# Kernel optimization log

Hardware: AMD Instinct MI355X
Metric: run time of the kernel (lower is better)

## Reference

```python
import jax, jax.numpy as jnp
import numpy as np

SEQ, H, VOCAB = 2048, 1024, 32000

def setup_inputs() -> dict:
    key = jax.random.key(0)
    ks = jax.random.split(key, 13)
    s = lambda k, shape, fan: jax.random.normal(k, shape, dtype=jnp.float32) / np.sqrt(fan)
    return {
        "word_input": jax.random.randint(ks[0], (1,), 0, VOCAB, dtype=jnp.int64),
        "last_context": s(ks[1], (1, H), H),
        "last_hidden": s(ks[2], (1, H), H),
        "encoder_outputs": s(ks[3], (SEQ, H), H),
        "emb": s(ks[4], (VOCAB, H), H),
        "W_ih": s(ks[5], (4 * H, 2 * H), 2 * H),
        "W_hh": s(ks[6], (4 * H, H), H),
        "b_ih": s(ks[7], (4 * H,), H),
        "b_hh": s(ks[8], (4 * H,), H),
        "Wa": s(ks[9], (H, H), H),
        "ba": s(ks[10], (H,), H),
        "Wl": s(ks[11], (VOCAB, 2 * H), 2 * H),
        "bl": s(ks[12], (VOCAB,), 2 * H),
    }

def reference(word_input, last_context, last_hidden, encoder_outputs,
              emb, W_ih, W_hh, b_ih, b_hh, Wa, ba, Wl, bl):
    # embedding lookup (batch=1, single step): [H]
    x = emb[word_input[0]]
    # rnn_input = cat(embedded, last_context): [2H]
    inp = jnp.concatenate([x, last_context[0]])
    h0 = last_hidden[0]
    c0 = jnp.zeros_like(h0)
    # single LSTM step, PyTorch gate order (i, f, g, o)
    gates = W_ih @ inp + b_ih + W_hh @ h0 + b_hh  # [4H]
    i_g, f_g, g_g, o_g = jnp.split(gates, 4)
    c = jax.nn.sigmoid(f_g) * c0 + jax.nn.sigmoid(i_g) * jnp.tanh(g_g)
    h = jax.nn.sigmoid(o_g) * jnp.tanh(c)  # lstm_output, [H]
    # Bahdanau-style scores: dot(h, Wa @ enc_i + ba) for each position (vectorized)
    energies = (encoder_outputs @ Wa.T + ba) @ h  # [SEQ]
    attn_w = jax.nn.softmax(energies)
    context = attn_w @ encoder_outputs  # [H]
    logits = Wl @ jnp.concatenate([h, context]) + bl  # [VOCAB]
    out = jax.nn.log_softmax(logits)
    return out[None, :]  # [1, VOCAB]
```

## Files before the change

### kernel.cpp

```cpp
#include <hip/hip_runtime.h>
#include <hip/hip_bf16.h>
#include <math.h>

#define SEQ   2048
#define H     1024
#define VOCAB 32000
#define GRID2 2048
#define NTHR  256

__device__ inline float4 ld4(const float* p) { return *reinterpret_cast<const float4*>(p); }
typedef float vfloat4 __attribute__((ext_vector_type(4)));
__device__ inline float4 ld4nt(const float* p) {
    vfloat4 v = __builtin_nontemporal_load(reinterpret_cast<const vfloat4*>(p));
    return make_float4(v.x, v.y, v.z, v.w);
}
__device__ inline float dot4(float4 a, float4 b) { return a.x*b.x + a.y*b.y + a.z*b.z + a.w*b.w; }
__device__ inline float sigmoidf(float x) { return 1.f / (1.f + expf(-x)); }

__device__ inline void omerge(float& m, float& s, float m2, float s2) {
    if (m2 > m) { s = s * __expf(m - m2) + s2; m = m2; }
    else if (s2 != 0.f) { s += s2 * __expf(m2 - m); }
}
__device__ inline float waveSum(float v) {
#pragma unroll
    for (int off = 32; off > 0; off >>= 1) v += __shfl_down(v, off, 64);
    return v;
}
__device__ inline void waveOmerge(float& m, float& s) {
#pragma unroll
    for (int off = 32; off > 0; off >>= 1) {
        float m2 = __shfl_down(m, off, 64), ss = __shfl_down(s, off, 64);
        omerge(m, s, m2, ss);
    }
}

__device__ inline void blockSignal(unsigned* f) {
    __syncthreads();
    if (threadIdx.x == 0) {
        __threadfence();
        __hip_atomic_fetch_add(f, 1u, __ATOMIC_RELEASE, __HIP_MEMORY_SCOPE_AGENT);
    }
}
__device__ inline void blockWait(unsigned* f, unsigned target) {
    if (threadIdx.x == 0) {
        while (__hip_atomic_load(f, __ATOMIC_ACQUIRE, __HIP_MEMORY_SCOPE_AGENT) < target)
            __builtin_amdgcn_s_sleep(4);
        __threadfence();
    }
    __syncthreads();
}


__global__ __launch_bounds__(NTHR) void k_init(float* __restrict__ ws) {
    const int t = threadIdx.x;
    unsigned* fl = (unsigned*)ws;
    if (t < 128) fl[t] = 0u;
    float* ctx = ws + 1152;
    float* u   = ws + 2176;
    for (int k = t; k < H; k += NTHR) { u[k] = 0.f; ctx[k] = 0.f; }
}

__global__ __launch_bounds__(NTHR, 8) void k_main(
        const float* __restrict__ emb,  const float* __restrict__ lctx,
        const float* __restrict__ h0,   const float* __restrict__ W_ih,
        const float* __restrict__ W_hh, const float* __restrict__ b_ih,
        const float* __restrict__ b_hh, const int* __restrict__ widx,
        const float* __restrict__ enc,  const float* __restrict__ Wa,
        const float* __restrict__ Wl,   const float* __restrict__ bl,
        float* __restrict__ ws, float* __restrict__ out) {
    const int bid = blockIdx.x, t = threadIdx.x;
    const int wid = t >> 6, lane = t & 63;

    unsigned* f_h   = (unsigned*)ws + 0;
    unsigned* f_u   = (unsigned*)ws + 16;
    unsigned* f_e   = (unsigned*)ws + 32;
    unsigned* f_ctx = (unsigned*)ws + 48;
    unsigned* f_l   = (unsigned*)ws + 64;
    float*  vcat   = ws + 128;
    float*  h      = vcat;
    float*  ctx    = vcat + H;
    float*  u      = ws + 2176;
    float*  energ  = ws + 3200;
    float2* part_e = (float2*)(ws + 5248);
    float2* part_l = (float2*)(ws + 5760);

    __shared__ float  lg[12];
    __shared__ float  shh[16];
    __shared__ float  se[8];
    __shared__ float  shw[32];
    __shared__ float2 s2[4];

    if (bid < 1024) {
        const int j = bid;
        const int w = widx[0];
        const float* xep = emb + (size_t)w * H;
        const float* wi = W_ih + (size_t)j * (2 * H);
        const float* wg = W_ih + (size_t)(j + 2 * H) * (2 * H);
        const float* wo = W_ih + (size_t)(j + 3 * H) * (2 * H);
        const float* vi = W_hh + (size_t)j * H;
        const float* vg = W_hh + (size_t)(j + 2 * H) * H;
        const float* vo = W_hh + (size_t)(j + 3 * H) * H;
        const int e = t * 4;
        float4 x0 = ld4(xep + e), x1 = ld4(lctx + e), x2 = ld4(h0 + e);
        float ai = dot4(ld4nt(wi + e), x0) + dot4(ld4nt(wi + H + e), x1) + dot4(ld4nt(vi + e), x2);
        float ag = dot4(ld4nt(wg + e), x0) + dot4(ld4nt(wg + H + e), x1) + dot4(ld4nt(vg + e), x2);
        float ao = dot4(ld4nt(wo + e), x0) + dot4(ld4nt(wo + H + e), x1) + dot4(ld4nt(vo + e), x2);
        ai = waveSum(ai); ag = waveSum(ag); ao = waveSum(ao);
        if (lane == 0) { lg[wid*3] = ai; lg[wid*3+1] = ag; lg[wid*3+2] = ao; }
        __syncthreads();
        if (t == 0) {
            float gi = 0.f, gg = 0.f, go = 0.f;
            for (int q = 0; q < 4; ++q) { gi += lg[q*3]; gg += lg[q*3+1]; go += lg[q*3+2]; }
            gi += b_ih[j] + b_hh[j];
            gg += b_ih[j + 2*H] + b_hh[j + 2*H];
            go += b_ih[j + 3*H] + b_hh[j + 3*H];
            float c = sigmoidf(gi) * tanhf(gg);
            h[j] = sigmoidf(go) * tanhf(c);
        }
        blockSignal(f_h);
    }

    blockWait(f_h, 1024);

    if (bid >= 1024 && bid < 1280) {
        const int ab = bid - 1024;
        {
            const int rg = ab >> 2, kb = ab & 3;
            if (t < 16) shh[t] = h[rg * 16 + t];
            __syncthreads();
            const int k = kb * 256 + t;
            float acc = 0.f;
#pragma unroll
            for (int jj = 0; jj < 16; ++jj)
                acc += Wa[(size_t)(rg * 16 + jj) * H + k] * shh[jj];
            atomicAdd(&u[k], acc);
            blockSignal(f_u);
            blockWait(f_u, 256);
        }
        {
#pragma unroll
            for (int rr = 0; rr < 2; ++rr) {
                const int row = ab * 8 + wid * 2 + rr;
                const float* er = enc + (size_t)row * H;
                float acc = 0.f;
#pragma unroll
                for (int it = 0; it < 4; ++it) {
                    const int e = it * 256 + lane * 4;
                    acc += dot4(ld4(er + e), ld4(u + e));
                }
                acc = waveSum(acc);
                if (lane == 0) { energ[row] = acc; se[wid * 2 + rr] = acc; }
            }
            __syncthreads();
            if (t == 0) {
                float m = -INFINITY, s = 0.f;
                for (int q = 0; q < 8; ++q) omerge(m, s, se[q], 1.f);
                part_e[ab] = make_float2(m, s);
            }
            blockSignal(f_e);
            blockWait(f_e, 256);
        }
        {
            float2 p = part_e[t];
            float m = p.x, s = p.y;
            waveOmerge(m, s);
            if (lane == 0) s2[wid] = make_float2(m, s);
            __syncthreads();
            float M = s2[0].x, S = s2[0].y;
#pragma unroll
            for (int q = 1; q < 4; ++q) omerge(M, S, s2[q].x, s2[q].y);
            const float invS = 1.f / S;
            const int rg = ab >> 2, kb = ab & 3;
            __syncthreads();
            if (t < 32) shw[t] = __expf(energ[rg * 32 + t] - M) * invS;
            __syncthreads();
            const int k = kb * 256 + t;
            float acc = 0.f;
#pragma unroll
            for (int jj = 0; jj < 32; ++jj)
                acc += shw[jj] * enc[(size_t)(rg * 32 + jj) * H + k];
            atomicAdd(&ctx[k], acc);
            blockSignal(f_ctx);
            blockWait(f_ctx, 256);
        }
        {
            const int aw = ab * 4 + wid;
            float4 xv[8];
#pragma unroll
            for (int q = 0; q < 8; ++q) xv[q] = ld4(vcat + q * 256 + lane * 4);
            float lm = -INFINITY, ls = 0.f;
#pragma unroll
            for (int rr = 0; rr < 4; ++rr) {
                if (rr < 3 || aw < 256) {
                    const int r = 28672 + aw + 1024 * rr;
                    const float* wr = Wl + (size_t)r * (2 * H);
                    float a = 0.f;
#pragma unroll
                    for (int q = 0; q < 8; ++q)
                        a += dot4(ld4(wr + q * 256 + lane * 4), xv[q]);
                    a = waveSum(a);
                    if (lane == 0) {
                        float v = a + bl[r];
                        out[r] = v;
                        omerge(lm, ls, v, 1.f);
                    }
                }
            }
            if (lane == 0) s2[wid] = make_float2(lm, ls);
            __syncthreads();
            if (t == 0) {
                float M = s2[0].x, S = s2[0].y;
#pragma unroll
                for (int q = 1; q < 4; ++q) omerge(M, S, s2[q].x, s2[q].y);
                part_l[bid] = make_float2(M, S);
            }
            blockSignal(f_l);
        }
    } else {
        const int sw = (bid < 1024) ? bid * 4 + wid : (bid - 256) * 4 + wid;
        const int r0 = sw * 4;
        float4 xv[4];
#pragma unroll
        for (int q = 0; q < 4; ++q) xv[q] = ld4(h + q * 256 + lane * 4);
        float acc4[4];
#pragma unroll
        for (int rr = 0; rr < 4; ++rr) {
            const float* wr = Wl + (size_t)(r0 + rr) * (2 * H);
            float a = 0.f;
#pragma unroll
            for (int q = 0; q < 4; ++q)
                a += dot4(ld4(wr + q * 256 + lane * 4), xv[q]);
            acc4[rr] = a;
        }
        blockWait(f_ctx, 256);
#pragma unroll
        for (int q = 0; q < 4; ++q) xv[q] = ld4(ctx + q * 256 + lane * 4);
        float lm = -INFINITY, ls = 0.f;
#pragma unroll
        for (int rr = 0; rr < 4; ++rr) {
            const int r = r0 + rr;
            const float* wr = Wl + (size_t)r * (2 * H) + H;
            float a = acc4[rr];
#pragma unroll
            for (int q = 0; q < 4; ++q)
                a += dot4(ld4(wr + q * 256 + lane * 4), xv[q]);
            a = waveSum(a);
            if (lane == 0) {
                float v = a + bl[r];
                out[r] = v;
                omerge(lm, ls, v, 1.f);
            }
        }
        if (lane == 0) s2[wid] = make_float2(lm, ls);
        __syncthreads();
        if (t == 0) {
            float M = s2[0].x, S = s2[0].y;
#pragma unroll
            for (int q = 1; q < 4; ++q) omerge(M, S, s2[q].x, s2[q].y);
            part_l[bid] = make_float2(M, S);
        }
        blockSignal(f_l);
    }

    if (bid < 125) {
        blockWait(f_l, 2048);
        float m = -INFINITY, s = 0.f;
#pragma unroll
        for (int q = 0; q < 8; ++q) {
            float2 p = part_l[t + q * 256];
            omerge(m, s, p.x, p.y);
        }
        waveOmerge(m, s);
        if (lane == 0) s2[wid] = make_float2(m, s);
        __syncthreads();
        float M = s2[0].x, S = s2[0].y;
#pragma unroll
        for (int q = 1; q < 4; ++q) omerge(M, S, s2[q].x, s2[q].y);
        const float lse = M + logf(S);
        const int i = bid * 256 + t;
        out[i] = out[i] - lse;
    }
}


__global__ __launch_bounds__(256) void k_lstm(
        const float* __restrict__ emb, const float* __restrict__ lctx,
        const float* __restrict__ h0,  const float* __restrict__ W_ih,
        const float* __restrict__ W_hh, const float* __restrict__ b_ih,
        const float* __restrict__ b_hh, const int* __restrict__ widx,
        float* __restrict__ h_out, float* __restrict__ u_zero,
        float* __restrict__ ctx_zero) {
    const int j = blockIdx.x, t = threadIdx.x;
    const int wid = t >> 6, lane = t & 63;
    if (j == 0) for (int k = t; k < H; k += 256) u_zero[k] = 0.f;
    if (j == 1) for (int k = t; k < H; k += 256) ctx_zero[k] = 0.f;
    const int w = widx[0];
    const float* embrow = emb + (size_t)w * H;
    const int ri = j, rg = j + 2 * H, ro = j + 3 * H;
    const float* wi_i = W_ih + (size_t)ri * (2 * H);
    const float* wi_g = W_ih + (size_t)rg * (2 * H);
    const float* wi_o = W_ih + (size_t)ro * (2 * H);
    const float* wh_i = W_hh + (size_t)ri * H;
    const float* wh_g = W_hh + (size_t)rg * H;
    const float* wh_o = W_hh + (size_t)ro * H;
    float ai = 0.f, ag = 0.f, ao = 0.f;
    { int e = t*4; float4 x = ld4(embrow+e);
      ai += dot4(ld4(wi_i+e),x); ag += dot4(ld4(wi_g+e),x); ao += dot4(ld4(wi_o+e),x); }
    { int e = t*4; float4 x = ld4(lctx+e);
      ai += dot4(ld4(wi_i+H+e),x); ag += dot4(ld4(wi_g+H+e),x); ao += dot4(ld4(wi_o+H+e),x); }
    { int e = t*4; float4 x = ld4(h0+e);
      ai += dot4(ld4(wh_i+e),x); ag += dot4(ld4(wh_g+e),x); ao += dot4(ld4(wh_o+e),x); }
    ai = waveSum(ai); ag = waveSum(ag); ao = waveSum(ao);
    __shared__ float lds[12];
    if (lane == 0) { lds[wid*3] = ai; lds[wid*3+1] = ag; lds[wid*3+2] = ao; }
    __syncthreads();
    if (t == 0) {
        float gi = 0.f, gg = 0.f, go = 0.f;
        for (int q = 0; q < 4; ++q) { gi += lds[q*3]; gg += lds[q*3+1]; go += lds[q*3+2]; }
        gi += b_ih[ri] + b_hh[ri];
        gg += b_ih[rg] + b_hh[rg];
        go += b_ih[ro] + b_hh[ro];
        float c = sigmoidf(gi) * tanhf(gg);
        h_out[j] = sigmoidf(go) * tanhf(c);
    }
}

__global__ __launch_bounds__(256) void k_wa(
        const float* __restrict__ Wa, const float* __restrict__ h,
        float* __restrict__ u) {
    const int k = blockIdx.x * 256 + threadIdx.x;
    const int j0 = blockIdx.y * 32;
    float acc = 0.f;
#pragma unroll 8
    for (int j = j0; j < j0 + 32; ++j) acc += Wa[(size_t)j * H + k] * h[j];
    atomicAdd(&u[k], acc);
}

__global__ __launch_bounds__(256) void k_energy(
        const float* __restrict__ enc, const float* __restrict__ u,
        float* __restrict__ energ, float2* __restrict__ part_e) {
    const int t = threadIdx.x, wid = t >> 6, lane = t & 63;
    const int row = blockIdx.x * 4 + wid;
    const float* er = enc + (size_t)row * H;
    float acc = 0.f;
#pragma unroll
    for (int it = 0; it < 4; ++it) { int e = it*256 + lane*4; acc += dot4(ld4(er+e), ld4(u+e)); }
    acc = waveSum(acc);
    __shared__ float se[4];
    if (lane == 0) { energ[row] = acc; se[wid] = acc; }
    __syncthreads();
    if (t == 0) {
        float m = fmaxf(fmaxf(se[0], se[1]), fmaxf(se[2], se[3]));
        float s = __expf(se[0]-m) + __expf(se[1]-m) + __expf(se[2]-m) + __expf(se[3]-m);
        part_e[blockIdx.x] = make_float2(m, s);
    }
}

__global__ __launch_bounds__(256) void k_ctx(
        const float* __restrict__ enc, const float* __restrict__ energ,
        const float2* __restrict__ part_e, float* __restrict__ ctx) {
    const int t = threadIdx.x, wid = t >> 6, lane = t & 63;
    __shared__ float2 s2[4];
    __shared__ float sh[64];
    float2 a = part_e[t], b = part_e[t + 256];
    float m = a.x, s = a.y;
    omerge(m, s, b.x, b.y);
    waveOmerge(m, s);
    if (lane == 0) s2[wid] = make_float2(m, s);
    __syncthreads();
    float M = s2[0].x, S = s2[0].y;
#pragma unroll
    for (int q = 1; q < 4; ++q) omerge(M, S, s2[q].x, s2[q].y);
    const float invS = 1.f / S;
    const int j0 = (blockIdx.x >> 2) * 64;
    __syncthreads();
    if (t < 64) sh[t] = __expf(energ[j0 + t] - M) * invS;
    __syncthreads();
    const int k = (blockIdx.x & 3) * 256 + t;
    float acc = 0.f;
#pragma unroll 8
    for (int jj = 0; jj < 64; ++jj) acc += sh[jj] * enc[(size_t)(j0 + jj) * H + k];
    atomicAdd(&ctx[k], acc);
}

__global__ __launch_bounds__(256) void k_logits(
        const float* __restrict__ Wl, const float* __restrict__ vcat,
        const float* __restrict__ bl, float* __restrict__ logits,
        float2* __restrict__ part_l) {
    const int t = threadIdx.x, wid = t >> 6, lane = t & 63;
    const int gw = blockIdx.x * 4 + wid;
    float4 xv[8];
#pragma unroll
    for (int q = 0; q < 8; ++q) xv[q] = ld4(vcat + q * 256 + lane * 4);
    float lm = -INFINITY, ls = 0.f;
#pragma unroll
    for (int rr = 0; rr < 4; ++rr) {
        const int row = gw * 4 + rr;
        const float* wr = Wl + (size_t)row * (2 * H);
        float acc = 0.f;
#pragma unroll
        for (int q = 0; q < 8; ++q)
            acc += dot4(ld4(wr + q * 256 + lane * 4), xv[q]);
        acc = waveSum(acc);
        if (lane == 0) {
            float v = acc + bl[row];
            logits[row] = v;
            omerge(lm, ls, v, 1.f);
        }
    }
    __shared__ float2 s2[4];
    if (lane == 0) s2[wid] = make_float2(lm, ls);
    __syncthreads();
    if (t == 0) {
        float M = s2[0].x, S = s2[0].y;
#pragma unroll
        for (int q = 1; q < 4; ++q) omerge(M, S, s2[q].x, s2[q].y);
        part_l[blockIdx.x] = make_float2(M, S);
    }
}

__global__ __launch_bounds__(256) void k_final(
        const float* __restrict__ logits, const float2* __restrict__ part_l,
        float* __restrict__ out) {
    const int t = threadIdx.x, wid = t >> 6, lane = t & 63;
    __shared__ float2 s2[4];
    float m = -INFINITY, s = 0.f;
    for (int i = t; i < 2000; i += 256) {
        float2 p = part_l[i];
        omerge(m, s, p.x, p.y);
    }
    waveOmerge(m, s);
    if (lane == 0) s2[wid] = make_float2(m, s);
    __syncthreads();
    float M = s2[0].x, S = s2[0].y;
#pragma unroll
    for (int q = 1; q < 4; ++q) omerge(M, S, s2[q].x, s2[q].y);
    const float lse = M + logf(S);
    const int i = blockIdx.x * 256 + t;
    out[i] = logits[i] - lse;
}

extern "C" void kernel_launch(void* const* d_in, const int* in_sizes, int n_in,
                              void* d_out, int out_size, void* d_ws, size_t ws_size,
                              hipStream_t stream) {
    const int*   widx = (const int*)d_in[0];
    const float* lctx = (const float*)d_in[1];
    const float* h0   = (const float*)d_in[2];
    const float* enc  = (const float*)d_in[3];
    const float* emb  = (const float*)d_in[4];
    const float* W_ih = (const float*)d_in[5];
    const float* W_hh = (const float*)d_in[6];
    const float* b_ih = (const float*)d_in[7];
    const float* b_hh = (const float*)d_in[8];
    const float* Wa   = (const float*)d_in[9];
    const float* Wl   = (const float*)d_in[11];
    const float* bl   = (const float*)d_in[12];
    float* out = (float*)d_out;
    float* ws  = (float*)d_ws;

    int occ = 0, nCU = 0, dev = 0;
    hipGetDevice(&dev);
    hipDeviceGetAttribute(&nCU, hipDeviceAttributeMultiprocessorCount, dev);
    hipError_t oe = hipOccupancyMaxActiveBlocksPerMultiprocessor(
        &occ, (const void*)k_main, NTHR, 0);
    const bool persistent_ok = (oe == hipSuccess) && ((long)occ * nCU >= GRID2);

    if (persistent_ok) {
        k_init<<<1, NTHR, 0, stream>>>(ws);
        k_main<<<GRID2, NTHR, 0, stream>>>(emb, lctx, h0, W_ih, W_hh, b_ih,
                                           b_hh, widx, enc, Wa, Wl, bl, ws, out);
    } else {
        float*  h      = ws;
        float*  ctx    = ws + 1024;
        float*  u      = ws + 2048;
        float*  energ  = ws + 3072;
        float2* part_e = (float2*)(ws + 5120);
        float2* part_l = (float2*)(ws + 6144);
        float*  logits = ws + 10240;
        k_lstm  <<<1024, 256, 0, stream>>>(emb, lctx, h0, W_ih, W_hh, b_ih, b_hh, widx, h, u, ctx);
        k_wa    <<<dim3(4, 32), 256, 0, stream>>>(Wa, h, u);
        k_energy<<<512, 256, 0, stream>>>(enc, u, energ, part_e);
        k_ctx   <<<128, 256, 0, stream>>>(enc, energ, part_e, ctx);
        k_logits<<<2000, 256, 0, stream>>>(Wl, ws , bl, logits, part_l);
        k_final <<<125, 256, 0, stream>>>(logits, part_l, out);
    }
}
```

Before: 74.47 us.

## Shard grid-barrier counters and use graduated backoff polling

```diff
diff --git a/kernel.cpp b/kernel.cpp
--- a/kernel.cpp
+++ b/kernel.cpp
@@ -9,11 +9,6 @@
 #define NTHR  256
 
 __device__ inline float4 ld4(const float* p) { return *reinterpret_cast<const float4*>(p); }
-typedef float vfloat4 __attribute__((ext_vector_type(4)));
-__device__ inline float4 ld4nt(const float* p) {
-    vfloat4 v = __builtin_nontemporal_load(reinterpret_cast<const vfloat4*>(p));
-    return make_float4(v.x, v.y, v.z, v.w);
-}
 __device__ inline float dot4(float4 a, float4 b) { return a.x*b.x + a.y*b.y + a.z*b.z + a.w*b.w; }
 __device__ inline float sigmoidf(float x) { return 1.f / (1.f + expf(-x)); }
 
@@ -34,17 +29,52 @@
     }
 }
 
-__device__ inline void blockSignal(unsigned* f) {
+#define SHARDS 16
+#define SHSTRIDE 32
+
+__device__ inline void blockSignalSh(unsigned* f) {
     __syncthreads();
     if (threadIdx.x == 0) {
         __threadfence();
-        __hip_atomic_fetch_add(f, 1u, __ATOMIC_RELEASE, __HIP_MEMORY_SCOPE_AGENT);
-    }
-}
-__device__ inline void blockWait(unsigned* f, unsigned target) {
+        __hip_atomic_fetch_add(&f[(blockIdx.x & (SHARDS - 1)) * SHSTRIDE], 1u,
+                               __ATOMIC_RELEASE, __HIP_MEMORY_SCOPE_AGENT);
+    }
+}
+__device__ inline unsigned shSum(unsigned* f) {
+    unsigned sum = 0;
+#pragma unroll
+    for (int q = 0; q < SHARDS; ++q)
+        sum += __hip_atomic_load(&f[q * SHSTRIDE], __ATOMIC_RELAXED,
+                                 __HIP_MEMORY_SCOPE_AGENT);
+    return sum;
+}
+__device__ inline void blockWaitSlow(unsigned* f, unsigned target) {
     if (threadIdx.x == 0) {
-        while (__hip_atomic_load(f, __ATOMIC_ACQUIRE, __HIP_MEMORY_SCOPE_AGENT) < target)
-            __builtin_amdgcn_s_sleep(4);
+        int it = 0;
+        while (shSum(f) < target) {
+            if (it < 2)       __builtin_amdgcn_s_sleep(1);
+            else if (it < 4)  __builtin_amdgcn_s_sleep(2);
+            else if (it < 6)  __builtin_amdgcn_s_sleep(4);
+            else if (it < 8)  __builtin_amdgcn_s_sleep(8);
+            else if (it < 10) __builtin_amdgcn_s_sleep(16);
+            else if (it < 12) __builtin_amdgcn_s_sleep(32);
+            else              __builtin_amdgcn_s_sleep(64);
+            ++it;
+        }
+        __threadfence();
+    }
+    __syncthreads();
+}
+__device__ inline void blockWaitFast(unsigned* f, unsigned target) {
+    if (threadIdx.x == 0) {
+        int it = 0;
+        while (shSum(f) < target) {
+            if (it < 2)      __builtin_amdgcn_s_sleep(1);
+            else if (it < 4) __builtin_amdgcn_s_sleep(2);
+            else if (it < 6) __builtin_amdgcn_s_sleep(4);
+            else             __builtin_amdgcn_s_sleep(8);
+            ++it;
+        }
         __threadfence();
     }
     __syncthreads();
@@ -54,9 +84,9 @@
 __global__ __launch_bounds__(NTHR) void k_init(float* __restrict__ ws) {
     const int t = threadIdx.x;
     unsigned* fl = (unsigned*)ws;
-    if (t < 128) fl[t] = 0u;
-    float* ctx = ws + 1152;
-    float* u   = ws + 2176;
+    for (int k = t; k < 2560; k += NTHR) fl[k] = 0u;
+    float* ctx = ws + 3584;
+    float* u   = ws + 4608;
     for (int k = t; k < H; k += NTHR) { u[k] = 0.f; ctx[k] = 0.f; }
 }
 
@@ -72,17 +102,17 @@
     const int wid = t >> 6, lane = t & 63;
 
     unsigned* f_h   = (unsigned*)ws + 0;
-    unsigned* f_u   = (unsigned*)ws + 16;
-    unsigned* f_e   = (unsigned*)ws + 32;
-    unsigned* f_ctx = (unsigned*)ws + 48;
-    unsigned* f_l   = (unsigned*)ws + 64;
-    float*  vcat   = ws + 128;
+    unsigned* f_u   = (unsigned*)ws + 512;
+    unsigned* f_e   = (unsigned*)ws + 1024;
+    unsigned* f_ctx = (unsigned*)ws + 1536;
+    unsigned* f_l   = (unsigned*)ws + 2048;
+    float*  vcat   = ws + 2560;
     float*  h      = vcat;
     float*  ctx    = vcat + H;
-    float*  u      = ws + 2176;
-    float*  energ  = ws + 3200;
-    float2* part_e = (float2*)(ws + 5248);
-    float2* part_l = (float2*)(ws + 5760);
+    float*  u      = ws + 4608;
+    float*  energ  = ws + 5632;
+    float2* part_e = (float2*)(ws + 7680);
+    float2* part_l = (float2*)(ws + 8192);
 
     __shared__ float  lg[12];
     __shared__ float  shh[16];
@@ -102,9 +132,9 @@
         const float* vo = W_hh + (size_t)(j + 3 * H) * H;
         const int e = t * 4;
         float4 x0 = ld4(xep + e), x1 = ld4(lctx + e), x2 = ld4(h0 + e);
-        float ai = dot4(ld4nt(wi + e), x0) + dot4(ld4nt(wi + H + e), x1) + dot4(ld4nt(vi + e), x2);
-        float ag = dot4(ld4nt(wg + e), x0) + dot4(ld4nt(wg + H + e), x1) + dot4(ld4nt(vg + e), x2);
-        float ao = dot4(ld4nt(wo + e), x0) + dot4(ld4nt(wo + H + e), x1) + dot4(ld4nt(vo + e), x2);
+        float ai = dot4(ld4(wi + e), x0) + dot4(ld4(wi + H + e), x1) + dot4(ld4(vi + e), x2);
+        float ag = dot4(ld4(wg + e), x0) + dot4(ld4(wg + H + e), x1) + dot4(ld4(vg + e), x2);
+        float ao = dot4(ld4(wo + e), x0) + dot4(ld4(wo + H + e), x1) + dot4(ld4(vo + e), x2);
         ai = waveSum(ai); ag = waveSum(ag); ao = waveSum(ao);
         if (lane == 0) { lg[wid*3] = ai; lg[wid*3+1] = ag; lg[wid*3+2] = ao; }
         __syncthreads();
@@ -117,10 +147,10 @@
             float c = sigmoidf(gi) * tanhf(gg);
             h[j] = sigmoidf(go) * tanhf(c);
         }
-        blockSignal(f_h);
-    }
-
-    blockWait(f_h, 1024);
+        blockSignalSh(f_h);
+    }
+
+    blockWaitSlow(f_h, 1024);
 
     if (bid >= 1024 && bid < 1280) {
         const int ab = bid - 1024;
@@ -134,8 +164,8 @@
             for (int jj = 0; jj < 16; ++jj)
                 acc += Wa[(size_t)(rg * 16 + jj) * H + k] * shh[jj];
             atomicAdd(&u[k], acc);
-            blockSignal(f_u);
-            blockWait(f_u, 256);
+            blockSignalSh(f_u);
+            blockWaitFast(f_u, 256);
         }
         {
 #pragma unroll
@@ -157,8 +187,8 @@
                 for (int q = 0; q < 8; ++q) omerge(m, s, se[q], 1.f);
                 part_e[ab] = make_float2(m, s);
             }
-            blockSignal(f_e);
-            blockWait(f_e, 256);
+            blockSignalSh(f_e);
+            blockWaitFast(f_e, 256);
         }
         {
             float2 p = part_e[t];
@@ -180,8 +210,8 @@
             for (int jj = 0; jj < 32; ++jj)
                 acc += shw[jj] * enc[(size_t)(rg * 32 + jj) * H + k];
             atomicAdd(&ctx[k], acc);
-            blockSignal(f_ctx);
-            blockWait(f_ctx, 256);
+            blockSignalSh(f_ctx);
+            blockWaitFast(f_ctx, 256);
         }
         {
             const int aw = ab * 4 + wid;
@@ -214,7 +244,7 @@
                 for (int q = 1; q < 4; ++q) omerge(M, S, s2[q].x, s2[q].y);
                 part_l[bid] = make_float2(M, S);
             }
-            blockSignal(f_l);
+            blockSignalSh(f_l);
         }
     } else {
         const int sw = (bid < 1024) ? bid * 4 + wid : (bid - 256) * 4 + wid;
@@ -232,7 +262,7 @@
                 a += dot4(ld4(wr + q * 256 + lane * 4), xv[q]);
             acc4[rr] = a;
         }
-        blockWait(f_ctx, 256);
+        blockWaitSlow(f_ctx, 256);
 #pragma unroll
         for (int q = 0; q < 4; ++q) xv[q] = ld4(ctx + q * 256 + lane * 4);
         float lm = -INFINITY, ls = 0.f;
@@ -259,11 +289,11 @@
             for (int q = 1; q < 4; ++q) omerge(M, S, s2[q].x, s2[q].y);
             part_l[bid] = make_float2(M, S);
         }
-        blockSignal(f_l);
+        blockSignalSh(f_l);
     }
 
     if (bid < 125) {
-        blockWait(f_l, 2048);
+        blockWaitSlow(f_l, 2048);
         float m = -INFINITY, s = 0.f;
 #pragma unroll
         for (int q = 0; q < 8; ++q) {
```

Measured after the change: 73.29 us. Within noise of the previous version (-1.6%).
